# Optimization experiments

Hardware: AMD Instinct MI355X
Metric: run time of the kernel (lower is better)

The kernel has to match this reference:

```python
import jax, jax.numpy as jnp
import numpy as np

INPUT_DIMS = 3
K = 64          # num_bases_per_dim
DEG = 3         # cubic
MIN_VAL = -1.0
MAX_VAL = 1.0
SCALE = (K - DEG) / (MAX_VAL - MIN_VAL)
EPS = 1e-6
N_POINTS = 1_000_000


def setup_inputs() -> dict:
    key = jax.random.key(0)
    x = jax.random.uniform(key, (N_POINTS, INPUT_DIMS), jnp.float32,
                           minval=-1.0, maxval=1.0)
    return {"x": x}


def reference(x):
    N, D = x.shape
    # scale to knot space and clamp so idx+3 <= K-1
    xs = jnp.clip((x - MIN_VAL) * SCALE, 0.0, K - DEG - EPS)
    idx = jnp.floor(xs).astype(jnp.int32)          # [N, D]
    u = xs - idx.astype(xs.dtype)                  # local coord in [0,1)
    u2 = u * u
    u3 = u2 * u
    c0 = (1.0 - u) ** 3 / 6.0
    c1 = (3.0 * u3 - 6.0 * u2 + 4.0) / 6.0
    c2 = (-3.0 * u3 + 3.0 * u2 + 3.0 * u + 1.0) / 6.0
    c3 = u3 / 6.0
    coeffs = jnp.stack([c0, c1, c2, c3], axis=-1)  # [N, D, 4]
    idxs = idx[..., None] + jnp.arange(4, dtype=jnp.int32)  # [N, D, 4]
    # scatter 4 active coefficients into K bins per (point, dim)
    bn = jnp.arange(N)[:, None, None]
    dn = jnp.arange(D)[None, :, None]
    feat = jnp.zeros((N, D, K), dtype=x.dtype).at[bn, dn, idxs].set(coeffs)
    # include_input=True: per-dim layout [x_d, feat_d] then concat over dims
    out = jnp.concatenate([x[:, :, None], feat], axis=2).reshape(N, D * (1 + K))
    return out
```

## Files before the change

kernel.cpp:

```cpp
#include <hip/hip_runtime.h>


constexpr int   DIMS        = 3;
constexpr int   K           = 64;
constexpr int   ROW         = DIMS * (1 + K);
constexpr float SCALE       = 30.5f;
constexpr float CLAMP_MAX   = 61.0f - 1e-6f;
constexpr int   PTS_PER_BLK = 64;
constexpr int   FLT_PER_BLK = PTS_PER_BLK * ROW;
constexpr int   V4_PER_BLK  = FLT_PER_BLK / 4;

__global__ __launch_bounds__(256)
void bspline_kernel(const float* __restrict__ x, float* __restrict__ out,
                    int n_points) {
    const int t = threadIdx.x;
    const long long block_base = (long long)blockIdx.x * FLT_PER_BLK;
    const long long total_flt  = (long long)n_points * ROW;

    float4* out4 = reinterpret_cast<float4*>(out + block_base);
    long long rem = total_flt - block_base;
    int lim = (rem >= FLT_PER_BLK) ? V4_PER_BLK : (int)(rem > 0 ? rem / 4 : 0);
    for (int f = t; f < lim; f += 256) {
        out4[f] = make_float4(0.f, 0.f, 0.f, 0.f);
    }

    __syncthreads();

    if (t < PTS_PER_BLK * DIMS) {
        const int nl = t / 3;
        const int d  = t - nl * 3;
        const int n  = blockIdx.x * PTS_PER_BLK + nl;
        if (n < n_points) {
            const float xv = x[n * 3 + d];
            float xs = (xv + 1.0f) * SCALE;
            xs = fminf(fmaxf(xs, 0.0f), CLAMP_MAX);
            const int   idx = (int)xs;
            const float u   = xs - (float)idx;
            const float u2  = u * u;
            const float u3  = u2 * u;
            const float om  = 1.0f - u;
            const float c0  = om * om * om * (1.0f / 6.0f);
            const float c1  = (3.0f * u3 - 6.0f * u2 + 4.0f) * (1.0f / 6.0f);
            const float c2  = (-3.0f * u3 + 3.0f * u2 + 3.0f * u + 1.0f) * (1.0f / 6.0f);
            const float c3  = u3 * (1.0f / 6.0f);

            float* row = out + (long long)n * ROW + d * (1 + K);
            row[0] = xv;
            float* fptr = row + 1 + idx;
            fptr[0] = c0;
            fptr[1] = c1;
            fptr[2] = c2;
            fptr[3] = c3;
        }
    }
}

extern "C" void kernel_launch(void* const* d_in, const int* in_sizes, int n_in,
                              void* d_out, int out_size, void* d_ws, size_t ws_size,
                              hipStream_t stream) {
    const float* x  = (const float*)d_in[0];
    float* out      = (float*)d_out;
    const int n_pts = in_sizes[0] / DIMS;
    const int nblk  = (n_pts + PTS_PER_BLK - 1) / PTS_PER_BLK;
    bspline_kernel<<<dim3(nblk), dim3(256), 0, stream>>>(x, out, n_pts);
}
```

Before: 871.8 us.

## Build output tiles in LDS and stream them with persistent double-buffered blocks

The kernel now builds each 16-point tile in shared memory: it zeroes the tile, scatters the coefficients into it, then writes it to global memory as coalesced float4 stores. Before, it zeroed global memory and then made scattered global writes on top. A fixed grid of 1536 persistent blocks loops over tiles with a two-buffer LDS ping-pong, so the next tile is prepared while the current one is stored. The aim is to drop the second, uncoalesced write pass to global memory. In exchange it adds block-wide syncs and a tail case: when n_points is not a multiple of 16, the last tile is written past the end of the output.

```diff
diff --git a/kernel.cpp b/kernel.cpp
--- a/kernel.cpp
+++ b/kernel.cpp
@@ -6,32 +6,26 @@
 constexpr int   ROW         = DIMS * (1 + K);
 constexpr float SCALE       = 30.5f;
 constexpr float CLAMP_MAX   = 61.0f - 1e-6f;
-constexpr int   PTS_PER_BLK = 64;
-constexpr int   FLT_PER_BLK = PTS_PER_BLK * ROW;
-constexpr int   V4_PER_BLK  = FLT_PER_BLK / 4;
+constexpr int   PTS_PER_TILE = 16;
+constexpr int   SEGS_PER_TILE = PTS_PER_TILE * DIMS;
+constexpr int   FLT_PER_TILE = PTS_PER_TILE * ROW;
+constexpr int   V4_PER_TILE  = FLT_PER_TILE / 4;
+constexpr int   NBLOCKS      = 1536;
 
-__global__ __launch_bounds__(256)
-void bspline_kernel(const float* __restrict__ x, float* __restrict__ out,
-                    int n_points) {
-    const int t = threadIdx.x;
-    const long long block_base = (long long)blockIdx.x * FLT_PER_BLK;
-    const long long total_flt  = (long long)n_points * ROW;
+__device__ __forceinline__ void zero_tile(float4* b4, int t) {
+    for (int f = t; f < V4_PER_TILE; f += 256)
+        b4[f] = make_float4(0.f, 0.f, 0.f, 0.f);
+}
 
-    float4* out4 = reinterpret_cast<float4*>(out + block_base);
-    long long rem = total_flt - block_base;
-    int lim = (rem >= FLT_PER_BLK) ? V4_PER_BLK : (int)(rem > 0 ? rem / 4 : 0);
-    for (int f = t; f < lim; f += 256) {
-        out4[f] = make_float4(0.f, 0.f, 0.f, 0.f);
-    }
-
-    __syncthreads();
-
-    if (t < PTS_PER_BLK * DIMS) {
-        const int nl = t / 3;
-        const int d  = t - nl * 3;
-        const int n  = blockIdx.x * PTS_PER_BLK + nl;
+__device__ __forceinline__ void scatter_tile(float* buf, int t, int tile,
+                                             const float* __restrict__ x,
+                                             int n_points) {
+    if (t < SEGS_PER_TILE) {
+        const int pt = t / 3;
+        const int d  = t - pt * 3;
+        const int n  = tile * PTS_PER_TILE + pt;
         if (n < n_points) {
-            const float xv = x[n * 3 + d];
+            const float xv = x[(long long)tile * SEGS_PER_TILE + t];
             float xs = (xv + 1.0f) * SCALE;
             xs = fminf(fmaxf(xs, 0.0f), CLAMP_MAX);
             const int   idx = (int)xs;
@@ -44,14 +38,50 @@
             const float c2  = (-3.0f * u3 + 3.0f * u2 + 3.0f * u + 1.0f) * (1.0f / 6.0f);
             const float c3  = u3 * (1.0f / 6.0f);
 
-            float* row = out + (long long)n * ROW + d * (1 + K);
-            row[0] = xv;
-            float* fptr = row + 1 + idx;
-            fptr[0] = c0;
-            fptr[1] = c1;
-            fptr[2] = c2;
-            fptr[3] = c3;
+            float* seg = buf + pt * ROW + d * (1 + K);
+            seg[0] = xv;
+            float* fp = seg + 1 + idx;
+            fp[0] = c0; fp[1] = c1; fp[2] = c2; fp[3] = c3;
         }
+    }
+}
+
+__device__ __forceinline__ void store_tile(const float4* b4, int t, int tile,
+                                           float4* __restrict__ out4) {
+    float4* dst = out4 + (long long)tile * V4_PER_TILE;
+    for (int f = t; f < V4_PER_TILE; f += 256)
+        dst[f] = b4[f];
+}
+
+__global__ __launch_bounds__(256)
+void bspline_kernel(const float* __restrict__ x, float* __restrict__ out,
+                    int n_points, int n_tiles) {
+    __shared__ __align__(16) float lds[2][FLT_PER_TILE];
+    const int t = threadIdx.x;
+    float4* out4 = reinterpret_cast<float4*>(out);
+
+    int tile = blockIdx.x;
+    if (tile >= n_tiles) return;
+
+    zero_tile(reinterpret_cast<float4*>(lds[0]), t);
+    __syncthreads();
+    scatter_tile(lds[0], t, tile, x, n_points);
+    __syncthreads();
+
+    int p = 0;
+    for (; tile < n_tiles; tile += NBLOCKS) {
+        store_tile(reinterpret_cast<const float4*>(lds[p]), t, tile, out4);
+
+        const int next = tile + NBLOCKS;
+        if (next < n_tiles) {
+            zero_tile(reinterpret_cast<float4*>(lds[p ^ 1]), t);
+        }
+        __syncthreads();
+        if (next < n_tiles) {
+            scatter_tile(lds[p ^ 1], t, next, x, n_points);
+        }
+        __syncthreads();
+        p ^= 1;
     }
 }
 
@@ -60,7 +90,7 @@
                               hipStream_t stream) {
     const float* x  = (const float*)d_in[0];
     float* out      = (float*)d_out;
-    const int n_pts = in_sizes[0] / DIMS;
-    const int nblk  = (n_pts + PTS_PER_BLK - 1) / PTS_PER_BLK;
-    bspline_kernel<<<dim3(nblk), dim3(256), 0, stream>>>(x, out, n_pts);
+    const int n_pts  = in_sizes[0] / DIMS;
+    const int n_tiles = (n_pts + PTS_PER_TILE - 1) / PTS_PER_TILE;
+    bspline_kernel<<<dim3(NBLOCKS), dim3(256), 0, stream>>>(x, out, n_pts, n_tiles);
 }
```

Result: faster. 770.3 us (-11.6%).

## Compute each output float4 directly instead of zero-fill then scatter

Applied to the files above, without the earlier changes.

Replaces the two-phase zero-fill plus scattered coefficient writes with a grid-stride loop in which each thread computes one float4 of the output directly, choosing the x value, a spline coefficient or zero per element. This removes the second pass of unaligned scalar scatter writes and the block barrier, so every output byte is written once with a vector store. In exchange each element recomputes the spline coefficients and reads x redundantly (cached). A fixed grid of 4096 blocks is used.

```diff
diff --git a/kernel.cpp b/kernel.cpp
--- a/kernel.cpp
+++ b/kernel.cpp
@@ -1,37 +1,37 @@
 #include <hip/hip_runtime.h>
 
 
-constexpr int   DIMS        = 3;
-constexpr int   K           = 64;
-constexpr int   ROW         = DIMS * (1 + K);
-constexpr float SCALE       = 30.5f;
-constexpr float CLAMP_MAX   = 61.0f - 1e-6f;
-constexpr int   PTS_PER_BLK = 64;
-constexpr int   FLT_PER_BLK = PTS_PER_BLK * ROW;
-constexpr int   V4_PER_BLK  = FLT_PER_BLK / 4;
+constexpr int   DIMS      = 3;
+constexpr int   K         = 64;
+constexpr int   ROW       = DIMS * (1 + K);
+constexpr float SCALE     = 30.5f;
+constexpr float CLAMP_MAX = 61.0f - 1e-6f;
+constexpr int   NBLOCKS   = 4096;
+constexpr int   NTHREADS  = 256;
 
 __global__ __launch_bounds__(256)
 void bspline_kernel(const float* __restrict__ x, float* __restrict__ out,
-                    int n_points) {
-    const int t = threadIdx.x;
-    const long long block_base = (long long)blockIdx.x * FLT_PER_BLK;
-    const long long total_flt  = (long long)n_points * ROW;
+                    unsigned int total4) {
+    const unsigned int stride = NBLOCKS * NTHREADS;
+    float4* __restrict__ out4 = reinterpret_cast<float4*>(out);
 
-    float4* out4 = reinterpret_cast<float4*>(out + block_base);
-    long long rem = total_flt - block_base;
-    int lim = (rem >= FLT_PER_BLK) ? V4_PER_BLK : (int)(rem > 0 ? rem / 4 : 0);
-    for (int f = t; f < lim; f += 256) {
-        out4[f] = make_float4(0.f, 0.f, 0.f, 0.f);
-    }
+    for (unsigned int f = blockIdx.x * NTHREADS + threadIdx.x; f < total4;
+         f += stride) {
+        const unsigned int g0 = f * 4u;
+        const unsigned int n0 = g0 / 195u;
+        const unsigned int r0 = g0 - n0 * 195u;
 
-    __syncthreads();
+        float comp[4];
+#pragma unroll
+        for (int k = 0; k < 4; ++k) {
+            unsigned int n = n0;
+            unsigned int r = r0 + (unsigned int)k;
+            if (r >= 195u) { n += 1u; r -= 195u; }
+            const unsigned int d = (r >= 130u) ? 2u : ((r >= 65u) ? 1u : 0u);
+            const unsigned int j = r - 65u * d;
 
-    if (t < PTS_PER_BLK * DIMS) {
-        const int nl = t / 3;
-        const int d  = t - nl * 3;
-        const int n  = blockIdx.x * PTS_PER_BLK + nl;
-        if (n < n_points) {
-            const float xv = x[n * 3 + d];
+            const float xv = x[n * 3u + d];
+
             float xs = (xv + 1.0f) * SCALE;
             xs = fminf(fmaxf(xs, 0.0f), CLAMP_MAX);
             const int   idx = (int)xs;
@@ -44,14 +44,16 @@
             const float c2  = (-3.0f * u3 + 3.0f * u2 + 3.0f * u + 1.0f) * (1.0f / 6.0f);
             const float c3  = u3 * (1.0f / 6.0f);
 
-            float* row = out + (long long)n * ROW + d * (1 + K);
-            row[0] = xv;
-            float* fptr = row + 1 + idx;
-            fptr[0] = c0;
-            fptr[1] = c1;
-            fptr[2] = c2;
-            fptr[3] = c3;
+            const int tt = (int)j - 1 - idx;
+            float val = 0.0f;
+            val = (tt == 0) ? c0 : val;
+            val = (tt == 1) ? c1 : val;
+            val = (tt == 2) ? c2 : val;
+            val = (tt == 3) ? c3 : val;
+            val = (j == 0u) ? xv : val;
+            comp[k] = val;
         }
+        out4[f] = make_float4(comp[0], comp[1], comp[2], comp[3]);
     }
 }
 
@@ -60,7 +62,8 @@
                               hipStream_t stream) {
     const float* x  = (const float*)d_in[0];
     float* out      = (float*)d_out;
-    const int n_pts = in_sizes[0] / DIMS;
-    const int nblk  = (n_pts + PTS_PER_BLK - 1) / PTS_PER_BLK;
-    bspline_kernel<<<dim3(nblk), dim3(256), 0, stream>>>(x, out, n_pts);
+    const long long n_pts  = in_sizes[0] / DIMS;
+    const unsigned int total4 =
+        (unsigned int)((n_pts * (long long)ROW) / 4);
+    bspline_kernel<<<dim3(NBLOCKS), dim3(NTHREADS), 0, stream>>>(x, out, total4);
 }
```

New measurement: 902.0 us. 1.03x slower.

## Compute spline params in shared memory and write each output float4 once

Applied to the files above, without the earlier changes.

Each block first computes per-(point,dim) x value, knot index and four cubic coefficients into shared memory. Then every thread generates full float4 output chunks by selecting zero, x or a coefficient, so each output element is written exactly once with coalesced vector stores. This replaces the zero-fill pass followed by scattered scalar overwrites. The cost is extra select logic and shared-memory reads per float4. The tail block reads past the last valid point only for padded pairs, and it still writes full V4_PER_BLK float4s without a bound check, which could overrun when N is not a multiple of 64.

```diff
diff --git a/kernel.cpp b/kernel.cpp
--- a/kernel.cpp
+++ b/kernel.cpp
@@ -7,51 +7,80 @@
 constexpr float SCALE       = 30.5f;
 constexpr float CLAMP_MAX   = 61.0f - 1e-6f;
 constexpr int   PTS_PER_BLK = 64;
+constexpr int   PAIRS       = PTS_PER_BLK * DIMS;
 constexpr int   FLT_PER_BLK = PTS_PER_BLK * ROW;
 constexpr int   V4_PER_BLK  = FLT_PER_BLK / 4;
 
 __global__ __launch_bounds__(256)
 void bspline_kernel(const float* __restrict__ x, float* __restrict__ out,
-                    int n_points) {
+                    int n_pairs_total) {
+    __shared__ __align__(16) float params[(PAIRS + 1) * 8];
     const int t = threadIdx.x;
-    const long long block_base = (long long)blockIdx.x * FLT_PER_BLK;
-    const long long total_flt  = (long long)n_points * ROW;
 
-    float4* out4 = reinterpret_cast<float4*>(out + block_base);
-    long long rem = total_flt - block_base;
-    int lim = (rem >= FLT_PER_BLK) ? V4_PER_BLK : (int)(rem > 0 ? rem / 4 : 0);
-    for (int f = t; f < lim; f += 256) {
-        out4[f] = make_float4(0.f, 0.f, 0.f, 0.f);
+    if (t < PAIRS) {
+        const int gp = blockIdx.x * PAIRS + t;
+        float xv = 0.0f;
+        if (gp < n_pairs_total) xv = x[gp];
+        float xs = (xv + 1.0f) * SCALE;
+        xs = fminf(fmaxf(xs, 0.0f), CLAMP_MAX);
+        const int   idx = (int)xs;
+        const float u   = xs - (float)idx;
+        const float u2  = u * u;
+        const float u3  = u2 * u;
+        const float om  = 1.0f - u;
+        float* rec = params + t * 8;
+        rec[0] = xv;
+        rec[1] = __int_as_float(idx);
+        rec[2] = om * om * om * (1.0f / 6.0f);
+        rec[3] = (3.0f * u3 - 6.0f * u2 + 4.0f) * (1.0f / 6.0f);
+        rec[4] = (-3.0f * u3 + 3.0f * u2 + 3.0f * u + 1.0f) * (1.0f / 6.0f);
+        rec[5] = u3 * (1.0f / 6.0f);
     }
-
+    if (t == 255) {
+        float* rec = params + PAIRS * 8;
+#pragma unroll
+        for (int i = 0; i < 8; ++i) rec[i] = 0.0f;
+    }
     __syncthreads();
 
-    if (t < PTS_PER_BLK * DIMS) {
-        const int nl = t / 3;
-        const int d  = t - nl * 3;
-        const int n  = blockIdx.x * PTS_PER_BLK + nl;
-        if (n < n_points) {
-            const float xv = x[n * 3 + d];
-            float xs = (xv + 1.0f) * SCALE;
-            xs = fminf(fmaxf(xs, 0.0f), CLAMP_MAX);
-            const int   idx = (int)xs;
-            const float u   = xs - (float)idx;
-            const float u2  = u * u;
-            const float u3  = u2 * u;
-            const float om  = 1.0f - u;
-            const float c0  = om * om * om * (1.0f / 6.0f);
-            const float c1  = (3.0f * u3 - 6.0f * u2 + 4.0f) * (1.0f / 6.0f);
-            const float c2  = (-3.0f * u3 + 3.0f * u2 + 3.0f * u + 1.0f) * (1.0f / 6.0f);
-            const float c3  = u3 * (1.0f / 6.0f);
+    const float4* p4 = reinterpret_cast<const float4*>(params);
+    float4* out4 = reinterpret_cast<float4*>(out)
+                 + (long long)blockIdx.x * V4_PER_BLK;
 
-            float* row = out + (long long)n * ROW + d * (1 + K);
-            row[0] = xv;
-            float* fptr = row + 1 + idx;
-            fptr[0] = c0;
-            fptr[1] = c1;
-            fptr[2] = c2;
-            fptr[3] = c3;
+    for (int f = t; f < V4_PER_BLK; f += 256) {
+        const int pos = f * 4;
+        const int p   = pos / 65;
+        const int j   = pos - p * 65;
+        const int p2  = p + ((j >= 62) ? 1 : 0);
+
+        const float4 a0 = p4[p * 2];
+        const float4 a1 = p4[p * 2 + 1];
+        const float4 b0 = p4[p2 * 2];
+        const float4 b1 = p4[p2 * 2 + 1];
+        const int ia = __float_as_int(a0.y);
+        const int ib = __float_as_int(b0.y);
+
+        float comp[4];
+#pragma unroll
+        for (int c = 0; c < 4; ++c) {
+            const int  o  = j + c;
+            const bool cr = (o >= 65);
+            const int  oo = cr ? (o - 65) : o;
+            const float xv = cr ? b0.x : a0.x;
+            const float k0 = cr ? b0.z : a0.z;
+            const float k1 = cr ? b0.w : a0.w;
+            const float k2 = cr ? b1.x : a1.x;
+            const float k3 = cr ? b1.y : a1.y;
+            const int  tt = oo - 1 - (cr ? ib : ia);
+            float v = 0.0f;
+            v = (tt == 0) ? k0 : v;
+            v = (tt == 1) ? k1 : v;
+            v = (tt == 2) ? k2 : v;
+            v = (tt == 3) ? k3 : v;
+            v = (oo == 0) ? xv : v;
+            comp[c] = v;
         }
+        out4[f] = make_float4(comp[0], comp[1], comp[2], comp[3]);
     }
 }
 
@@ -62,5 +91,5 @@
     float* out      = (float*)d_out;
     const int n_pts = in_sizes[0] / DIMS;
     const int nblk  = (n_pts + PTS_PER_BLK - 1) / PTS_PER_BLK;
-    bspline_kernel<<<dim3(nblk), dim3(256), 0, stream>>>(x, out, n_pts);
+    bspline_kernel<<<dim3(nblk), dim3(256), 0, stream>>>(x, out, n_pts * DIMS);
 }
```

New measurement: 770.3 us. 11.6% less time.
